# Kernel tuning notes

Hardware: AMD Instinct MI355X
Metric: run time of the kernel (lower is better)

Reference implementation:

```python
import jax, jax.numpy as jnp
import numpy as np

ALPHA = 0.2  # LeakyReLU negative slope


def _gat_layer(x, W, a):
    """One GraphAttentionLayer (concat=True -> elu output).
    x: (B,N,Din); W: (Din,F); a: (2F,1).
    Faithful to source: adj mask is computed then discarded (softmax over raw e),
    so adj does not enter the math. Uses the additive decomposition
    e_ij = leakyrelu(a1.h_i + a2.h_j) which is mathematically identical to the
    dense (N,N,2F) concat in the original.
    """
    h = x @ W                      # (B,N,F)
    F = W.shape[1]
    a1, a2 = a[:F, 0], a[F:, 0]    # (F,), (F,)
    f1 = h @ a1                    # (B,N)
    f2 = h @ a2                    # (B,N)
    e = jax.nn.leaky_relu(f1[:, :, None] + f2[:, None, :], negative_slope=ALPHA)  # (B,N,N)
    att = jax.nn.softmax(e, axis=-1)
    h_prime = jnp.einsum('bnm,bmf->bnf', att, h)
    return jax.nn.elu(h_prime)


def setup_inputs() -> dict:
    key = jax.random.key(0)
    ks = jax.random.split(key, 6)
    B, N, D, H, F = 8, 1024, 256, 8, 128
    x = jax.random.normal(ks[0], (B, N, D), jnp.float32)
    adj = (jax.random.uniform(ks[1], (N, N)) > 0.9).astype(jnp.float32)
    xavier = lambda fi, fo: 1.414 * (2.0 / (fi + fo)) ** 0.5
    W_heads = jax.random.normal(ks[2], (H, D, F), jnp.float32) * xavier(D, F)
    a_heads = jax.random.normal(ks[3], (H, 2 * F, 1), jnp.float32) * xavier(2 * F, 1)
    W_out = jax.random.normal(ks[4], (H * F, F), jnp.float32) * xavier(H * F, F)
    a_out = jax.random.normal(ks[5], (2 * F, 1), jnp.float32) * xavier(2 * F, 1)
    return {"x": x, "adj": adj, "W_heads": W_heads, "a_heads": a_heads,
            "W_out": W_out, "a_out": a_out}


def reference(x, adj, W_heads, a_heads, W_out, a_out):
    # GAT.forward (dropout omitted: eval mode identity). adj unused per source bug.
    heads = jax.vmap(lambda W, a: _gat_layer(x, W, a))(W_heads, a_heads)  # (H,B,N,F)
    B, N = x.shape[0], x.shape[1]
    xc = jnp.transpose(heads, (1, 2, 0, 3)).reshape(B, N, -1)  # concat heads: (B,N,H*F)
    # out_att has concat=True (applies elu), then GAT.forward applies elu again.
    return jax.nn.elu(_gat_layer(xc, W_out, a_out))
```

## Files before the change

kernel.cpp:

```cpp
#include <hip/hip_runtime.h>
#include <math.h>

#define ALPHA 0.2f
#define LOG2E 1.44269504089f

typedef __attribute__((ext_vector_type(8))) short bf16x8;
typedef __attribute__((ext_vector_type(4))) float f32x4;

__device__ __forceinline__ float elu1(float x)  { return x > 0.f ? x : (__expf(x) - 1.f); }

__device__ __forceinline__ unsigned short f2bf(float x) {
    unsigned u = __float_as_uint(x);
    return (unsigned short)((u + 0x7fffu + ((u >> 16) & 1u)) >> 16);
}
__device__ __forceinline__ unsigned pkbf16(float a, float b) {
    return (unsigned)f2bf(a) | ((unsigned)f2bf(b) << 16);
}
__device__ __forceinline__ float bflo(unsigned v) { return __uint_as_float(v << 16); }
__device__ __forceinline__ float bfhi(unsigned v) { return __uint_as_float(v & 0xffff0000u); }
__device__ __forceinline__ float bfs(unsigned short v) { return __uint_as_float((unsigned)v << 16); }
__device__ __forceinline__ unsigned pkbf_rhu(float a, float b) {
    unsigned ua = __float_as_uint(a) + 0x8000u;
    unsigned ub = __float_as_uint(b) + 0x8000u;
    return __builtin_amdgcn_perm(ub, ua, 0x07060302u);
}

__global__ __launch_bounds__(256) void cvt_w_all(
    const float* __restrict__ Wh, const float* __restrict__ Wo,
    unsigned short* __restrict__ WhT, unsigned short* __restrict__ WoT)
{
    const int z = blockIdx.z;
    const int K = (z < 8) ? 256 : 1024;
    if (blockIdx.x * 64 >= K) return;
    const float* in = (z < 8) ? (Wh + (size_t)z * K * 128) : Wo;
    unsigned short* out = (z < 8) ? (WhT + (size_t)z * 128 * K) : WoT;

    __shared__ float T[64][65];
    const int tid = threadIdx.x;
    const int k0 = blockIdx.x * 64, n0 = blockIdx.y * 64;

    const int kr = tid >> 4, nc = (tid & 15) * 4;
#pragma unroll
    for (int s = 0; s < 4; ++s) {
        float4 v = *(const float4*)(in + (size_t)(k0 + kr + s * 16) * 128 + n0 + nc);
        T[kr + s * 16][nc]     = v.x;
        T[kr + s * 16][nc + 1] = v.y;
        T[kr + s * 16][nc + 2] = v.z;
        T[kr + s * 16][nc + 3] = v.w;
    }
    __syncthreads();
    const int nr0 = tid >> 3, kc = (tid & 7) * 8;
#pragma unroll
    for (int s = 0; s < 2; ++s) {
        int nr = nr0 + s * 32;
        unsigned pk[4];
#pragma unroll
        for (int q = 0; q < 4; ++q)
            pk[q] = pkbf16(T[kc + 2 * q][nr], T[kc + 2 * q + 1][nr]);
        *(uint4*)(out + (size_t)(n0 + nr) * K + k0 + kc) = make_uint4(pk[0], pk[1], pk[2], pk[3]);
    }
}

template <int BM, int BN, int WM, int WN, int DOF, int AF32>
__global__ __launch_bounds__(256) void gemm_t(
    const void* __restrict__ Avp, const unsigned short* __restrict__ Bt,
    unsigned short* __restrict__ Ct, int K,
    const float* __restrict__ aV, float* __restrict__ f1g, float* __restrict__ f2g)
{
    const int RM = WM / 16, RN = WN / 16;
    const int NCA = BM * 8 / 256, NCB = BN * 8 / 256;
    __shared__ __align__(16) unsigned short SAB[(BM + BN) * 72];
    unsigned short (*As)[72] = (unsigned short(*)[72])SAB;
    unsigned short (*Bs)[72] = (unsigned short(*)[72])(SAB + BM * 72);
    unsigned short (*Cs)[BM + 8] = (unsigned short(*)[BM + 8])SAB;
    float* redf = (float*)(SAB + BN * (BM + 8));

    const int tid = threadIdx.x;
    const int w = tid >> 6, lane = tid & 63;
    const int n16 = lane & 15, quad = lane >> 4;
    const int WX = BM / WM;
    const int wm = (w % WX) * WM, wn = (w / WX) * WN;
    const int m0 = blockIdx.x * BM, n0 = blockIdx.y * BN;

    const float* Af = (const float*)Avp;
    const unsigned short* Ab = (const unsigned short*)Avp;
    const int ar = tid >> 2, akc = (tid & 3) * 16;

    f32x4 acc[RM][RN];
#pragma unroll
    for (int mm = 0; mm < RM; ++mm)
#pragma unroll
        for (int nn = 0; nn < RN; ++nn) acc[mm][nn] = (f32x4){0.f, 0.f, 0.f, 0.f};

    uint4 ra[NCA], rb[NCB];
    float4 raf[4];
    if (AF32) {
#pragma unroll
        for (int j = 0; j < 4; ++j)
            raf[j] = *(const float4*)(Af + (size_t)(m0 + ar) * K + akc + 4 * j);
    } else {
#pragma unroll
        for (int i = 0; i < NCA; ++i) {
            int c = tid * NCA + i, r = c >> 3, cc = (c & 7) * 8;
            ra[i] = *(const uint4*)(Ab + (size_t)(m0 + r) * K + cc);
        }
    }
#pragma unroll
    for (int i = 0; i < NCB; ++i) {
        int c = tid * NCB + i, r = c >> 3, cc = (c & 7) * 8;
        rb[i] = *(const uint4*)(Bt + (size_t)(n0 + r) * K + cc);
    }

    const int nk = K >> 6;
    for (int kt = 0; kt < nk; ++kt) {
        __syncthreads();
        if (AF32) {
            uint4 lo = make_uint4(pkbf16(raf[0].x, raf[0].y), pkbf16(raf[0].z, raf[0].w),
                                  pkbf16(raf[1].x, raf[1].y), pkbf16(raf[1].z, raf[1].w));
            uint4 hi = make_uint4(pkbf16(raf[2].x, raf[2].y), pkbf16(raf[2].z, raf[2].w),
                                  pkbf16(raf[3].x, raf[3].y), pkbf16(raf[3].z, raf[3].w));
            *(uint4*)&As[ar][akc]     = lo;
            *(uint4*)&As[ar][akc + 8] = hi;
        } else {
#pragma unroll
            for (int i = 0; i < NCA; ++i) {
                int c = tid * NCA + i, r = c >> 3, cc = (c & 7) * 8;
                *(uint4*)&As[r][cc] = ra[i];
            }
        }
#pragma unroll
        for (int i = 0; i < NCB; ++i) {
            int c = tid * NCB + i, r = c >> 3, cc = (c & 7) * 8;
            *(uint4*)&Bs[r][cc] = rb[i];
        }
        __syncthreads();
        if (kt + 1 < nk) {
            int k0 = (kt + 1) * 64;
            if (AF32) {
#pragma unroll
                for (int j = 0; j < 4; ++j)
                    raf[j] = *(const float4*)(Af + (size_t)(m0 + ar) * K + k0 + akc + 4 * j);
            } else {
#pragma unroll
                for (int i = 0; i < NCA; ++i) {
                    int c = tid * NCA + i, r = c >> 3, cc = (c & 7) * 8;
                    ra[i] = *(const uint4*)(Ab + (size_t)(m0 + r) * K + k0 + cc);
                }
            }
#pragma unroll
            for (int i = 0; i < NCB; ++i) {
                int c = tid * NCB + i, r = c >> 3, cc = (c & 7) * 8;
                rb[i] = *(const uint4*)(Bt + (size_t)(n0 + r) * K + k0 + cc);
            }
        }
#pragma unroll
        for (int ks = 0; ks < 2; ++ks) {
            bf16x8 am[RM], bn[RN];
#pragma unroll
            for (int mm = 0; mm < RM; ++mm)
                am[mm] = *(const bf16x8*)&As[wm + mm * 16 + n16][ks * 32 + quad * 8];
#pragma unroll
            for (int nn = 0; nn < RN; ++nn)
                bn[nn] = *(const bf16x8*)&Bs[wn + nn * 16 + n16][ks * 32 + quad * 8];
#pragma unroll
            for (int mm = 0; mm < RM; ++mm)
#pragma unroll
                for (int nn = 0; nn < RN; ++nn)
                    acc[mm][nn] = __builtin_amdgcn_mfma_f32_16x16x32_bf16(
                        am[mm], bn[nn], acc[mm][nn], 0, 0, 0);
        }
    }

    __syncthreads();

#pragma unroll
    for (int nn = 0; nn < RN; ++nn) {
        int n = wn + nn * 16 + n16;
#pragma unroll
        for (int mm = 0; mm < RM; ++mm) {
            int m = wm + mm * 16 + quad * 4;
            f32x4 a = acc[mm][nn];
            ushort4 o = make_ushort4(f2bf(a[0]), f2bf(a[1]), f2bf(a[2]), f2bf(a[3]));
            *(ushort4*)&Cs[n][m] = o;
        }
    }
    __syncthreads();

    const int CHUNKS = BM * 2 / 16;
    const int RPP = 256 / CHUNKS;
    const int row = tid / CHUNKS, ch = tid % CHUNKS;
#pragma unroll
    for (int s = 0; s < BN / RPP; ++s) {
        int n = row + s * RPP;
        *(uint4*)(Ct + (size_t)(n0 + n) * 8192 + m0 + ch * 8) =
            *(const uint4*)&Cs[n][ch * 8];
    }

    if (DOF) {
        const int G = 256 / BM;
        const int FP = 128 / G;
        const int mloc = tid % BM, fq = tid / BM;
        const float* az = aV + blockIdx.y * 256;
        float s1 = 0.f, s2 = 0.f;
#pragma unroll 8
        for (int k = 0; k < FP; ++k) {
            int f = fq * FP + k;
            float h = bfs(Cs[f][mloc]);
            s1 += h * az[f];
            s2 += h * az[128 + f];
        }
        *(float2*)&redf[(fq * BM + mloc) * 2] = make_float2(s1, s2);
        __syncthreads();
        if (tid < BM) {
            float a1 = 0.f, a2 = 0.f;
#pragma unroll
            for (int g = 0; g < G; ++g) {
                a1 += redf[(g * BM + tid) * 2];
                a2 += redf[(g * BM + tid) * 2 + 1];
            }
            f1g[(size_t)blockIdx.y * 8192 + m0 + tid] = a1;
            f2g[(size_t)blockIdx.y * 8192 + m0 + tid] = a2;
        }
    }
}

template <int NI, int OUTBF, int NT>
__global__ __launch_bounds__(256) void attn4(
    const unsigned short* __restrict__ hT, const float* __restrict__ f1g,
    const float* __restrict__ f2g, float* __restrict__ outf,
    unsigned short* __restrict__ outb, int elu2)
{
    const int N = 1024, JT = 64, JP = 72;
    __shared__ __align__(16) unsigned short hls[2][NT * 16][JP];
    __shared__ float ul[1024], vl[1024];
    __shared__ float wred[4];

    const int tid = threadIdx.x;
    const int w = tid >> 6, lane = tid & 63;
    const int n16 = lane & 15, quad = lane >> 4;
    const int hy = OUTBF ? blockIdx.x : 0;
    const int bz = OUTBF ? blockIdx.z : blockIdx.x;
    const int fz = OUTBF ? 0 : blockIdx.z;
    const int ibx = blockIdx.y;
    const int hb = hy * 8 + bz;
    const int ITILE = 64 * NI;
    const int iw0 = ibx * ITILE + w * (16 * NI);

    const int j4 = tid * 4;
    {
        float4 fv = *(const float4*)(f2g + (size_t)hb * N + j4);
        fv.x *= LOG2E; fv.y *= LOG2E; fv.z *= LOG2E; fv.w *= LOG2E;
        *(float4*)&ul[j4] = fv;
        float m4 = fmaxf(fmaxf(fv.x, fv.y), fmaxf(fv.z, fv.w));
#pragma unroll
        for (int off = 32; off; off >>= 1) m4 = fmaxf(m4, __shfl_xor(m4, off));
        if (lane == 0) wred[w] = m4;
    }

    float f1L[NI];
#pragma unroll
    for (int ii = 0; ii < NI; ++ii)
        f1L[ii] = f1g[(size_t)hb * N + iw0 + ii * 16 + n16] * LOG2E;

    const unsigned short* gsrc = hT + (size_t)(hy * 128 + fz * (NT * 16)) * 8192 + bz * 1024;
    const int sf = tid >> 3, sj = (tid & 7) * 8;

    bf16x8 stg[NT / 2];
#pragma unroll
    for (int s = 0; s < NT / 2; ++s)
        stg[s] = *(const bf16x8*)(gsrc + (size_t)(sf + 32 * s) * 8192 + sj);

    __syncthreads();
    const float f2mL = fmaxf(fmaxf(wred[0], wred[1]), fmaxf(wred[2], wred[3]));

    {
        float4 raw = *(const float4*)&ul[j4];
        float4 uu, vv;
        float d0 = raw.x - f2mL, d1 = raw.y - f2mL, d2 = raw.z - f2mL, d3 = raw.w - f2mL;
        uu.x = __builtin_amdgcn_exp2f(d0); vv.x = __builtin_amdgcn_exp2f(ALPHA * d0);
        uu.y = __builtin_amdgcn_exp2f(d1); vv.y = __builtin_amdgcn_exp2f(ALPHA * d1);
        uu.z = __builtin_amdgcn_exp2f(d2); vv.z = __builtin_amdgcn_exp2f(ALPHA * d2);
        uu.w = __builtin_amdgcn_exp2f(d3); vv.w = __builtin_amdgcn_exp2f(ALPHA * d3);
        *(float4*)&ul[j4] = uu;
        *(float4*)&vl[j4] = vv;
    }

    float ri[NI];
#pragma unroll
    for (int ii = 0; ii < NI; ++ii)
        ri[ii] = __builtin_amdgcn_exp2f((ALPHA - 1.f) * (f1L[ii] + f2mL));

    f32x4 acc[NI][NT], accl[NI];
#pragma unroll
    for (int ii = 0; ii < NI; ++ii) {
        accl[ii] = (f32x4){0.f, 0.f, 0.f, 0.f};
#pragma unroll
        for (int t = 0; t < NT; ++t) acc[ii][t] = (f32x4){0.f, 0.f, 0.f, 0.f};
    }
    bf16x8 ones;
    { union { bf16x8 v; unsigned u[4]; } o;
      o.u[0] = o.u[1] = o.u[2] = o.u[3] = 0x3F803F80u; ones = o.v; }

#pragma unroll
    for (int s = 0; s < NT / 2; ++s)
        *(bf16x8*)&hls[0][sf + 32 * s][sj] = stg[s];
    __syncthreads();

    for (int jt = 0; jt < N / JT; ++jt) {
        const int cur = jt & 1;
        if (jt + 1 < N / JT) {
            int j0n = (jt + 1) * JT;
#pragma unroll
            for (int s = 0; s < NT / 2; ++s)
                stg[s] = *(const bf16x8*)(gsrc + (size_t)(sf + 32 * s) * 8192 + j0n + sj);
        }
        const int j0 = jt * JT;
#pragma unroll
        for (int kk = 0; kk < 2; ++kk) {
            const int jb = j0 + kk * 32 + quad * 8;
            float4 u0 = *(const float4*)&ul[jb], u1 = *(const float4*)&ul[jb + 4];
            float4 v0 = *(const float4*)&vl[jb], v1 = *(const float4*)&vl[jb + 4];
            float uj[8] = {u0.x, u0.y, u0.z, u0.w, u1.x, u1.y, u1.z, u1.w};
            float vj[8] = {v0.x, v0.y, v0.z, v0.w, v1.x, v1.y, v1.z, v1.w};

            bf16x8 afr[NI];
#pragma unroll
            for (int ii = 0; ii < NI; ++ii) {
                union { bf16x8 v; unsigned u[4]; } cvt;
#pragma unroll
                for (int q = 0; q < 4; ++q) {
                    float p0 = fmaxf(uj[2 * q],     ri[ii] * vj[2 * q]);
                    float p1 = fmaxf(uj[2 * q + 1], ri[ii] * vj[2 * q + 1]);
                    cvt.u[q] = pkbf_rhu(p0, p1);
                }
                afr[ii] = cvt.v;
            }
#pragma unroll
            for (int t = 0; t < NT; ++t) {
                bf16x8 bfr = *(const bf16x8*)&hls[cur][t * 16 + n16][kk * 32 + quad * 8];
#pragma unroll
                for (int ii = 0; ii < NI; ++ii)
                    acc[ii][t] = __builtin_amdgcn_mfma_f32_16x16x32_bf16(
                        afr[ii], bfr, acc[ii][t], 0, 0, 0);
            }
#pragma unroll
            for (int ii = 0; ii < NI; ++ii)
                accl[ii] = __builtin_amdgcn_mfma_f32_16x16x32_bf16(
                    afr[ii], ones, accl[ii], 0, 0, 0);
        }
        if (jt + 1 < N / JT) {
#pragma unroll
            for (int s = 0; s < NT / 2; ++s)
                *(bf16x8*)&hls[1 - cur][sf + 32 * s][sj] = stg[s];
        }
        __syncthreads();
    }

#pragma unroll
    for (int ii = 0; ii < NI; ++ii) {
#pragma unroll
        for (int r = 0; r < 4; ++r) {
            float inv = 1.f / accl[ii][r];
            int i = iw0 + ii * 16 + quad * 4 + r;
#pragma unroll
            for (int t = 0; t < NT; ++t) {
                float tv = acc[ii][t][r] * inv;
                tv = elu1(tv);
                if (OUTBF) {
                    outb[(size_t)(bz * 1024 + i) * 1024 + hy * 128 + t * 16 + n16] = f2bf(tv);
                } else {
                    if (elu2) tv = elu1(tv);
                    outf[(size_t)(bz * 1024 + i) * 128 + fz * (NT * 16) + t * 16 + n16] = tv;
                }
            }
        }
    }
}

extern "C" void kernel_launch(void* const* d_in, const int* in_sizes, int n_in,
                              void* d_out, int out_size, void* d_ws, size_t ws_size,
                              hipStream_t stream)
{
    const float* x  = (const float*)d_in[0];
    const float* Wh = (const float*)d_in[2];
    const float* ah = (const float*)d_in[3];
    const float* Wo = (const float*)d_in[4];
    const float* ao = (const float*)d_in[5];
    float* out = (float*)d_out;

    unsigned short* WhT = (unsigned short*)d_ws;
    unsigned short* WoT = WhT + 262144;
    unsigned short* h1T = WoT + 131072;
    unsigned short* xcb = h1T + 8388608;
    unsigned short* h2T = xcb + 8388608;
    float* f1a  = (float*)(h2T + 1048576);
    float* f2a  = f1a + 65536;
    float* f1b  = f2a + 65536;
    float* f2b  = f1b + 8192;

    cvt_w_all<<<dim3(16, 2, 9), 256, 0, stream>>>(Wh, Wo, WhT, WoT);

    gemm_t<64, 128, 32, 64, 1, 1><<<dim3(128, 8), 256, 0, stream>>>(
        x, WhT, h1T, 256, ah, f1a, f2a);
    attn4<2, 1, 8><<<dim3(8, 8, 8), 256, 0, stream>>>(h1T, f1a, f2a, nullptr, xcb, 0);

    gemm_t<32, 128, 16, 64, 1, 0><<<dim3(256, 1), 256, 0, stream>>>(
        xcb, WoT, h2T, 1024, ao, f1b, f2b);
    attn4<1, 0, 4><<<dim3(8, 16, 2), 256, 0, stream>>>(h2T, f1b, f2b, out, nullptr, 1);
}
```

Before: 167.1 us.

## Pre-convert x to bf16, widen head attention blocks, stage bf16 output via LDS

The weight-conversion kernel now also converts x to bf16, so the first projection GEMM reads a bf16 input instead of fp32. The first attention kernel runs 512-thread blocks covering twice as many query rows. Each staged key/value tile is therefore reused across more rows, and the grid is halved. Its bf16 output is written through an LDS transpose buffer and stored as coalesced 16-byte rows instead of scattered 2-byte stores. The trade-offs are an extra global pass over x, larger blocks that may lower occupancy, and added block syncs in the epilogue.

```diff
diff --git a/kernel.cpp b/kernel.cpp
--- a/kernel.cpp
+++ b/kernel.cpp
@@ -27,16 +27,27 @@
 
 __global__ __launch_bounds__(256) void cvt_w_all(
     const float* __restrict__ Wh, const float* __restrict__ Wo,
-    unsigned short* __restrict__ WhT, unsigned short* __restrict__ WoT)
+    const float* __restrict__ xf,
+    unsigned short* __restrict__ WhT, unsigned short* __restrict__ WoT,
+    unsigned short* __restrict__ xbf)
 {
     const int z = blockIdx.z;
+    const int tid = threadIdx.x;
+    if (z >= 9) {
+        size_t idx = ((((size_t)(z - 9) * 2 + blockIdx.y) * 16) + blockIdx.x) * 2048
+                   + (size_t)tid * 8;
+        float4 a = *(const float4*)(xf + idx);
+        float4 b = *(const float4*)(xf + idx + 4);
+        *(uint4*)(xbf + idx) = make_uint4(pkbf16(a.x, a.y), pkbf16(a.z, a.w),
+                                          pkbf16(b.x, b.y), pkbf16(b.z, b.w));
+        return;
+    }
     const int K = (z < 8) ? 256 : 1024;
     if (blockIdx.x * 64 >= K) return;
     const float* in = (z < 8) ? (Wh + (size_t)z * K * 128) : Wo;
     unsigned short* out = (z < 8) ? (WhT + (size_t)z * 128 * K) : WoT;
 
     __shared__ float T[64][65];
-    const int tid = threadIdx.x;
     const int k0 = blockIdx.x * 64, n0 = blockIdx.y * 64;
 
     const int kr = tid >> 4, nc = (tid & 15) * 4;
@@ -224,16 +235,20 @@
     }
 }
 
-template <int NI, int OUTBF, int NT>
-__global__ __launch_bounds__(256) void attn4(
+template <int NI, int OUTBF, int NT, int THREADS>
+__global__ __launch_bounds__(THREADS) void attn4(
     const unsigned short* __restrict__ hT, const float* __restrict__ f1g,
     const float* __restrict__ f2g, float* __restrict__ outf,
     unsigned short* __restrict__ outb, int elu2)
 {
     const int N = 1024, JT = 64, JP = 72;
+    const int NW = THREADS / 64;
+    const int ITILE = 16 * NI * NW;
+    const int NTS = NT * 16 * 8 / THREADS;
+    const int SR = THREADS / 8;
     __shared__ __align__(16) unsigned short hls[2][NT * 16][JP];
     __shared__ float ul[1024], vl[1024];
-    __shared__ float wred[4];
+    __shared__ float wred[NW];
 
     const int tid = threadIdx.x;
     const int w = tid >> 6, lane = tid & 63;
@@ -243,11 +258,10 @@
     const int fz = OUTBF ? 0 : blockIdx.z;
     const int ibx = blockIdx.y;
     const int hb = hy * 8 + bz;
-    const int ITILE = 64 * NI;
     const int iw0 = ibx * ITILE + w * (16 * NI);
 
-    const int j4 = tid * 4;
-    {
+    if (THREADS == 256) {
+        const int j4 = tid * 4;
         float4 fv = *(const float4*)(f2g + (size_t)hb * N + j4);
         fv.x *= LOG2E; fv.y *= LOG2E; fv.z *= LOG2E; fv.w *= LOG2E;
         *(float4*)&ul[j4] = fv;
@@ -255,6 +269,15 @@
 #pragma unroll
         for (int off = 32; off; off >>= 1) m4 = fmaxf(m4, __shfl_xor(m4, off));
         if (lane == 0) wred[w] = m4;
+    } else {
+        const int j2 = tid * 2;
+        float2 fv = *(const float2*)(f2g + (size_t)hb * N + j2);
+        fv.x *= LOG2E; fv.y *= LOG2E;
+        *(float2*)&ul[j2] = fv;
+        float m4 = fmaxf(fv.x, fv.y);
+#pragma unroll
+        for (int off = 32; off; off >>= 1) m4 = fmaxf(m4, __shfl_xor(m4, off));
+        if (lane == 0) wred[w] = m4;
     }
 
     float f1L[NI];
@@ -265,15 +288,18 @@
     const unsigned short* gsrc = hT + (size_t)(hy * 128 + fz * (NT * 16)) * 8192 + bz * 1024;
     const int sf = tid >> 3, sj = (tid & 7) * 8;
 
-    bf16x8 stg[NT / 2];
-#pragma unroll
-    for (int s = 0; s < NT / 2; ++s)
-        stg[s] = *(const bf16x8*)(gsrc + (size_t)(sf + 32 * s) * 8192 + sj);
+    bf16x8 stg[NTS];
+#pragma unroll
+    for (int s = 0; s < NTS; ++s)
+        stg[s] = *(const bf16x8*)(gsrc + (size_t)(sf + SR * s) * 8192 + sj);
 
     __syncthreads();
-    const float f2mL = fmaxf(fmaxf(wred[0], wred[1]), fmaxf(wred[2], wred[3]));
-
-    {
+    float f2mL = wred[0];
+#pragma unroll
+    for (int k = 1; k < NW; ++k) f2mL = fmaxf(f2mL, wred[k]);
+
+    if (THREADS == 256) {
+        const int j4 = tid * 4;
         float4 raw = *(const float4*)&ul[j4];
         float4 uu, vv;
         float d0 = raw.x - f2mL, d1 = raw.y - f2mL, d2 = raw.z - f2mL, d3 = raw.w - f2mL;
@@ -283,6 +309,15 @@
         uu.w = __builtin_amdgcn_exp2f(d3); vv.w = __builtin_amdgcn_exp2f(ALPHA * d3);
         *(float4*)&ul[j4] = uu;
         *(float4*)&vl[j4] = vv;
+    } else {
+        const int j2 = tid * 2;
+        float2 raw = *(const float2*)&ul[j2];
+        float d0 = raw.x - f2mL, d1 = raw.y - f2mL;
+        float2 uu, vv;
+        uu.x = __builtin_amdgcn_exp2f(d0); vv.x = __builtin_amdgcn_exp2f(ALPHA * d0);
+        uu.y = __builtin_amdgcn_exp2f(d1); vv.y = __builtin_amdgcn_exp2f(ALPHA * d1);
+        *(float2*)&ul[j2] = uu;
+        *(float2*)&vl[j2] = vv;
     }
 
     float ri[NI];
@@ -302,8 +337,8 @@
       o.u[0] = o.u[1] = o.u[2] = o.u[3] = 0x3F803F80u; ones = o.v; }
 
 #pragma unroll
-    for (int s = 0; s < NT / 2; ++s)
-        *(bf16x8*)&hls[0][sf + 32 * s][sj] = stg[s];
+    for (int s = 0; s < NTS; ++s)
+        *(bf16x8*)&hls[0][sf + SR * s][sj] = stg[s];
     __syncthreads();
 
     for (int jt = 0; jt < N / JT; ++jt) {
@@ -311,8 +346,8 @@
         if (jt + 1 < N / JT) {
             int j0n = (jt + 1) * JT;
 #pragma unroll
-            for (int s = 0; s < NT / 2; ++s)
-                stg[s] = *(const bf16x8*)(gsrc + (size_t)(sf + 32 * s) * 8192 + j0n + sj);
+            for (int s = 0; s < NTS; ++s)
+                stg[s] = *(const bf16x8*)(gsrc + (size_t)(sf + SR * s) * 8192 + j0n + sj);
         }
         const int j0 = jt * JT;
 #pragma unroll
@@ -350,25 +385,56 @@
         }
         if (jt + 1 < N / JT) {
 #pragma unroll
-            for (int s = 0; s < NT / 2; ++s)
-                *(bf16x8*)&hls[1 - cur][sf + 32 * s][sj] = stg[s];
+            for (int s = 0; s < NTS; ++s)
+                *(bf16x8*)&hls[1 - cur][sf + SR * s][sj] = stg[s];
         }
         __syncthreads();
     }
 
-#pragma unroll
-    for (int ii = 0; ii < NI; ++ii) {
-#pragma unroll
-        for (int r = 0; r < 4; ++r) {
-            float inv = 1.f / accl[ii][r];
-            int i = iw0 + ii * 16 + quad * 4 + r;
-#pragma unroll
-            for (int t = 0; t < NT; ++t) {
-                float tv = acc[ii][t][r] * inv;
-                tv = elu1(tv);
-                if (OUTBF) {
-                    outb[(size_t)(bz * 1024 + i) * 1024 + hy * 128 + t * 16 + n16] = f2bf(tv);
-                } else {
+    if (OUTBF) {
+        unsigned short (*Os)[140] = (unsigned short(*)[140])hls;
+        const int WPP = 128 / (16 * NI);
+#pragma unroll
+        for (int pass = 0; pass < ITILE / 128; ++pass) {
+            __syncthreads();
+            if ((w / WPP) == pass) {
+#pragma unroll
+                for (int ii = 0; ii < NI; ++ii)
+#pragma unroll
+                    for (int r = 0; r < 4; ++r) {
+                        float inv = 1.f / accl[ii][r];
+                        int il = (w % WPP) * (16 * NI) + ii * 16 + quad * 4 + r;
+#pragma unroll
+                        for (int t = 0; t < NT; ++t)
+                            Os[il][t * 16 + n16] = f2bf(elu1(acc[ii][t][r] * inv));
+                    }
+            }
+            __syncthreads();
+            {
+                int orow = tid >> 2, q4 = tid & 3;
+                size_t gb = (size_t)(bz * 1024 + ibx * ITILE + pass * 128 + orow) * 1024
+                          + hy * 128 + q4 * 32;
+                uint2 d[8];
+#pragma unroll
+                for (int s = 0; s < 8; ++s)
+                    d[s] = *(const uint2*)&Os[orow][q4 * 32 + s * 4];
+                *(uint4*)(outb + gb)      = make_uint4(d[0].x, d[0].y, d[1].x, d[1].y);
+                *(uint4*)(outb + gb + 8)  = make_uint4(d[2].x, d[2].y, d[3].x, d[3].y);
+                *(uint4*)(outb + gb + 16) = make_uint4(d[4].x, d[4].y, d[5].x, d[5].y);
+                *(uint4*)(outb + gb + 24) = make_uint4(d[6].x, d[6].y, d[7].x, d[7].y);
+            }
+        }
+    } else {
+#pragma unroll
+        for (int ii = 0; ii < NI; ++ii) {
+#pragma unroll
+            for (int r = 0; r < 4; ++r) {
+                float inv = 1.f / accl[ii][r];
+                int i = iw0 + ii * 16 + quad * 4 + r;
+#pragma unroll
+                for (int t = 0; t < NT; ++t) {
+                    float tv = acc[ii][t][r] * inv;
+                    tv = elu1(tv);
                     if (elu2) tv = elu1(tv);
                     outf[(size_t)(bz * 1024 + i) * 128 + fz * (NT * 16) + t * 16 + n16] = tv;
                 }
@@ -397,14 +463,15 @@
     float* f2a  = f1a + 65536;
     float* f1b  = f2a + 65536;
     float* f2b  = f1b + 8192;
-
-    cvt_w_all<<<dim3(16, 2, 9), 256, 0, stream>>>(Wh, Wo, WhT, WoT);
-
-    gemm_t<64, 128, 32, 64, 1, 1><<<dim3(128, 8), 256, 0, stream>>>(
-        x, WhT, h1T, 256, ah, f1a, f2a);
-    attn4<2, 1, 8><<<dim3(8, 8, 8), 256, 0, stream>>>(h1T, f1a, f2a, nullptr, xcb, 0);
+    unsigned short* xbf = (unsigned short*)(f2b + 8192);
+
+    cvt_w_all<<<dim3(16, 2, 41), 256, 0, stream>>>(Wh, Wo, x, WhT, WoT, xbf);
+
+    gemm_t<64, 128, 32, 64, 1, 0><<<dim3(128, 8), 256, 0, stream>>>(
+        xbf, WhT, h1T, 256, ah, f1a, f2a);
+    attn4<2, 1, 8, 512><<<dim3(8, 4, 8), 512, 0, stream>>>(h1T, f1a, f2a, nullptr, xcb, 0);
 
     gemm_t<32, 128, 16, 64, 1, 0><<<dim3(256, 1), 256, 0, stream>>>(
         xcb, WoT, h2T, 1024, ao, f1b, f2b);
-    attn4<1, 0, 4><<<dim3(8, 16, 2), 256, 0, stream>>>(h2T, f1b, f2b, out, nullptr, 1);
-}
+    attn4<1, 0, 4, 256><<<dim3(8, 16, 2), 256, 0, stream>>>(h2T, f1b, f2b, out, nullptr, 1);
+}
```

After: 181.0 us. 8.3% more time.

## Stage full 64-feature h slice in LDS and widen attention and GEMM blocks

Applied to the files above, without the earlier changes.

The attention kernel now loads the whole 64x1024 bf16 slice of h into LDS once (about 129 KB) and drops the double-buffered 64-column j-tile pipeline and its per-tile barriers. Each block covers 64 output features instead of 128 or 64, and the first layer uses 512-thread blocks with four i-rows per warp. The first GEMM also moves to 128x128 tiles with 512 threads. The goal is to remove per-tile sync and staging overhead and to reuse each h slice across more rows. In exchange, the large LDS footprint limits occupancy to about one block per CU, and the initial load is no longer overlapped with compute.

```diff
diff --git a/kernel.cpp b/kernel.cpp
--- a/kernel.cpp
+++ b/kernel.cpp
@@ -16,8 +16,6 @@
 __device__ __forceinline__ unsigned pkbf16(float a, float b) {
     return (unsigned)f2bf(a) | ((unsigned)f2bf(b) << 16);
 }
-__device__ __forceinline__ float bflo(unsigned v) { return __uint_as_float(v << 16); }
-__device__ __forceinline__ float bfhi(unsigned v) { return __uint_as_float(v & 0xffff0000u); }
 __device__ __forceinline__ float bfs(unsigned short v) { return __uint_as_float((unsigned)v << 16); }
 __device__ __forceinline__ unsigned pkbf_rhu(float a, float b) {
     unsigned ua = __float_as_uint(a) + 0x8000u;
@@ -61,15 +59,18 @@
     }
 }
 
-template <int BM, int BN, int WM, int WN, int DOF, int AF32>
-__global__ __launch_bounds__(256) void gemm_t(
+template <int BM, int BN, int WM, int WN, int DOF, int AF32, int THREADS>
+__global__ __launch_bounds__(THREADS) void gemm_t(
     const void* __restrict__ Avp, const unsigned short* __restrict__ Bt,
     unsigned short* __restrict__ Ct, int K,
     const float* __restrict__ aV, float* __restrict__ f1g, float* __restrict__ f2g)
 {
     const int RM = WM / 16, RN = WN / 16;
-    const int NCA = BM * 8 / 256, NCB = BN * 8 / 256;
-    __shared__ __align__(16) unsigned short SAB[(BM + BN) * 72];
+    const int NCA = BM * 8 / THREADS, NCB = BN * 8 / THREADS;
+    constexpr int SAB_A = (BM + BN) * 72;
+    constexpr int SAB_B = BN * (BM + 8) + THREADS * 4;
+    constexpr int SAB_SH = SAB_A > SAB_B ? SAB_A : SAB_B;
+    __shared__ __align__(16) unsigned short SAB[SAB_SH];
     unsigned short (*As)[72] = (unsigned short(*)[72])SAB;
     unsigned short (*Bs)[72] = (unsigned short(*)[72])(SAB + BM * 72);
     unsigned short (*Cs)[BM + 8] = (unsigned short(*)[BM + 8])SAB;
@@ -92,7 +93,7 @@
 #pragma unroll
         for (int nn = 0; nn < RN; ++nn) acc[mm][nn] = (f32x4){0.f, 0.f, 0.f, 0.f};
 
-    uint4 ra[NCA], rb[NCB];
+    uint4 ra[NCA ? NCA : 1], rb[NCB];
     float4 raf[4];
     if (AF32) {
 #pragma unroll
@@ -187,7 +188,7 @@
     __syncthreads();
 
     const int CHUNKS = BM * 2 / 16;
-    const int RPP = 256 / CHUNKS;
+    const int RPP = THREADS / CHUNKS;
     const int row = tid / CHUNKS, ch = tid % CHUNKS;
 #pragma unroll
     for (int s = 0; s < BN / RPP; ++s) {
@@ -197,7 +198,7 @@
     }
 
     if (DOF) {
-        const int G = 256 / BM;
+        const int G = THREADS / BM;
         const int FP = 128 / G;
         const int mloc = tid % BM, fq = tid / BM;
         const float* az = aV + blockIdx.y * 256;
@@ -224,30 +225,31 @@
     }
 }
 
-template <int NI, int OUTBF, int NT>
-__global__ __launch_bounds__(256) void attn4(
+template <int NI, int OUTBF, int THREADS>
+__global__ __launch_bounds__(THREADS) void attn6(
     const unsigned short* __restrict__ hT, const float* __restrict__ f1g,
     const float* __restrict__ f2g, float* __restrict__ outf,
-    unsigned short* __restrict__ outb, int elu2)
+    unsigned short* __restrict__ outb)
 {
-    const int N = 1024, JT = 64, JP = 72;
-    __shared__ __align__(16) unsigned short hls[2][NT * 16][JP];
+    const int N = 1024;
+    const int NW = THREADS / 64;
+    const int ITILE = NW * 16 * NI;
+    const int EPT = 1024 / THREADS;
+    __shared__ __align__(16) unsigned short hfull[64][1032];
     __shared__ float ul[1024], vl[1024];
-    __shared__ float wred[4];
+    __shared__ float wred[NW];
 
     const int tid = threadIdx.x;
     const int w = tid >> 6, lane = tid & 63;
     const int n16 = lane & 15, quad = lane >> 4;
-    const int hy = OUTBF ? blockIdx.x : 0;
-    const int bz = OUTBF ? blockIdx.z : blockIdx.x;
-    const int fz = OUTBF ? 0 : blockIdx.z;
-    const int ibx = blockIdx.y;
+    int hy, bz, ibx, fz;
+    if (OUTBF) { hy = blockIdx.x; ibx = blockIdx.y; bz = blockIdx.z >> 1; fz = blockIdx.z & 1; }
+    else       { hy = 0; bz = blockIdx.x; ibx = blockIdx.y; fz = blockIdx.z; }
     const int hb = hy * 8 + bz;
-    const int ITILE = 64 * NI;
     const int iw0 = ibx * ITILE + w * (16 * NI);
 
-    const int j4 = tid * 4;
-    {
+    if (EPT == 4) {
+        const int j4 = tid * 4;
         float4 fv = *(const float4*)(f2g + (size_t)hb * N + j4);
         fv.x *= LOG2E; fv.y *= LOG2E; fv.z *= LOG2E; fv.w *= LOG2E;
         *(float4*)&ul[j4] = fv;
@@ -255,6 +257,15 @@
 #pragma unroll
         for (int off = 32; off; off >>= 1) m4 = fmaxf(m4, __shfl_xor(m4, off));
         if (lane == 0) wred[w] = m4;
+    } else {
+        const int j2 = tid * 2;
+        float2 fv = *(const float2*)(f2g + (size_t)hb * N + j2);
+        fv.x *= LOG2E; fv.y *= LOG2E;
+        *(float2*)&ul[j2] = fv;
+        float m4 = fmaxf(fv.x, fv.y);
+#pragma unroll
+        for (int off = 32; off; off >>= 1) m4 = fmaxf(m4, __shfl_xor(m4, off));
+        if (lane == 0) wred[w] = m4;
     }
 
     float f1L[NI];
@@ -262,18 +273,24 @@
     for (int ii = 0; ii < NI; ++ii)
         f1L[ii] = f1g[(size_t)hb * N + iw0 + ii * 16 + n16] * LOG2E;
 
-    const unsigned short* gsrc = hT + (size_t)(hy * 128 + fz * (NT * 16)) * 8192 + bz * 1024;
-    const int sf = tid >> 3, sj = (tid & 7) * 8;
-
-    bf16x8 stg[NT / 2];
-#pragma unroll
-    for (int s = 0; s < NT / 2; ++s)
-        stg[s] = *(const bf16x8*)(gsrc + (size_t)(sf + 32 * s) * 8192 + sj);
+    const unsigned short* gsrc = hT + (size_t)(hy * 128 + fz * 64) * 8192 + bz * 1024;
+    const int sr = tid >> 3;
+    const int sc = (tid & 7) * 8;
+    const int SRW = THREADS / 8;
+#pragma unroll
+    for (int s = 0; s < 64 / SRW; ++s)
+#pragma unroll
+        for (int c = 0; c < 16; ++c)
+            *(bf16x8*)&hfull[sr + SRW * s][sc + c * 64] =
+                *(const bf16x8*)(gsrc + (size_t)(sr + SRW * s) * 8192 + sc + c * 64);
 
     __syncthreads();
-    const float f2mL = fmaxf(fmaxf(wred[0], wred[1]), fmaxf(wred[2], wred[3]));
-
-    {
+    float f2mL = wred[0];
+#pragma unroll
+    for (int k = 1; k < NW; ++k) f2mL = fmaxf(f2mL, wred[k]);
+
+    if (EPT == 4) {
+        const int j4 = tid * 4;
         float4 raw = *(const float4*)&ul[j4];
         float4 uu, vv;
         float d0 = raw.x - f2mL, d1 = raw.y - f2mL, d2 = raw.z - f2mL, d3 = raw.w - f2mL;
@@ -283,6 +300,15 @@
         uu.w = __builtin_amdgcn_exp2f(d3); vv.w = __builtin_amdgcn_exp2f(ALPHA * d3);
         *(float4*)&ul[j4] = uu;
         *(float4*)&vl[j4] = vv;
+    } else {
+        const int j2 = tid * 2;
+        float2 raw = *(const float2*)&ul[j2];
+        float d0 = raw.x - f2mL, d1 = raw.y - f2mL;
+        float2 uu, vv;
+        uu.x = __builtin_amdgcn_exp2f(d0); vv.x = __builtin_amdgcn_exp2f(ALPHA * d0);
+        uu.y = __builtin_amdgcn_exp2f(d1); vv.y = __builtin_amdgcn_exp2f(ALPHA * d1);
+        *(float2*)&ul[j2] = uu;
+        *(float2*)&vl[j2] = vv;
     }
 
     float ri[NI];
@@ -290,70 +316,50 @@
     for (int ii = 0; ii < NI; ++ii)
         ri[ii] = __builtin_amdgcn_exp2f((ALPHA - 1.f) * (f1L[ii] + f2mL));
 
-    f32x4 acc[NI][NT], accl[NI];
+    f32x4 acc[NI][4], accl[NI];
 #pragma unroll
     for (int ii = 0; ii < NI; ++ii) {
         accl[ii] = (f32x4){0.f, 0.f, 0.f, 0.f};
 #pragma unroll
-        for (int t = 0; t < NT; ++t) acc[ii][t] = (f32x4){0.f, 0.f, 0.f, 0.f};
+        for (int t = 0; t < 4; ++t) acc[ii][t] = (f32x4){0.f, 0.f, 0.f, 0.f};
     }
     bf16x8 ones;
     { union { bf16x8 v; unsigned u[4]; } o;
       o.u[0] = o.u[1] = o.u[2] = o.u[3] = 0x3F803F80u; ones = o.v; }
 
-#pragma unroll
-    for (int s = 0; s < NT / 2; ++s)
-        *(bf16x8*)&hls[0][sf + 32 * s][sj] = stg[s];
     __syncthreads();
 
-    for (int jt = 0; jt < N / JT; ++jt) {
-        const int cur = jt & 1;
-        if (jt + 1 < N / JT) {
-            int j0n = (jt + 1) * JT;
-#pragma unroll
-            for (int s = 0; s < NT / 2; ++s)
-                stg[s] = *(const bf16x8*)(gsrc + (size_t)(sf + 32 * s) * 8192 + j0n + sj);
-        }
-        const int j0 = jt * JT;
-#pragma unroll
-        for (int kk = 0; kk < 2; ++kk) {
-            const int jb = j0 + kk * 32 + quad * 8;
-            float4 u0 = *(const float4*)&ul[jb], u1 = *(const float4*)&ul[jb + 4];
-            float4 v0 = *(const float4*)&vl[jb], v1 = *(const float4*)&vl[jb + 4];
-            float uj[8] = {u0.x, u0.y, u0.z, u0.w, u1.x, u1.y, u1.z, u1.w};
-            float vj[8] = {v0.x, v0.y, v0.z, v0.w, v1.x, v1.y, v1.z, v1.w};
-
-            bf16x8 afr[NI];
-#pragma unroll
-            for (int ii = 0; ii < NI; ++ii) {
-                union { bf16x8 v; unsigned u[4]; } cvt;
-#pragma unroll
-                for (int q = 0; q < 4; ++q) {
-                    float p0 = fmaxf(uj[2 * q],     ri[ii] * vj[2 * q]);
-                    float p1 = fmaxf(uj[2 * q + 1], ri[ii] * vj[2 * q + 1]);
-                    cvt.u[q] = pkbf_rhu(p0, p1);
-                }
-                afr[ii] = cvt.v;
-            }
-#pragma unroll
-            for (int t = 0; t < NT; ++t) {
-                bf16x8 bfr = *(const bf16x8*)&hls[cur][t * 16 + n16][kk * 32 + quad * 8];
-#pragma unroll
-                for (int ii = 0; ii < NI; ++ii)
-                    acc[ii][t] = __builtin_amdgcn_mfma_f32_16x16x32_bf16(
-                        afr[ii], bfr, acc[ii][t], 0, 0, 0);
-            }
+    for (int kk = 0; kk < 32; ++kk) {
+        const int jb = kk * 32 + quad * 8;
+        float4 u0 = *(const float4*)&ul[jb], u1 = *(const float4*)&ul[jb + 4];
+        float4 v0 = *(const float4*)&vl[jb], v1 = *(const float4*)&vl[jb + 4];
+        float uj[8] = {u0.x, u0.y, u0.z, u0.w, u1.x, u1.y, u1.z, u1.w};
+        float vj[8] = {v0.x, v0.y, v0.z, v0.w, v1.x, v1.y, v1.z, v1.w};
+
+        bf16x8 afr[NI];
+#pragma unroll
+        for (int ii = 0; ii < NI; ++ii) {
+            union { bf16x8 v; unsigned u[4]; } cvt;
+#pragma unroll
+            for (int q = 0; q < 4; ++q) {
+                float p0 = fmaxf(uj[2 * q],     ri[ii] * vj[2 * q]);
+                float p1 = fmaxf(uj[2 * q + 1], ri[ii] * vj[2 * q + 1]);
+                cvt.u[q] = pkbf_rhu(p0, p1);
+            }
+            afr[ii] = cvt.v;
+        }
+#pragma unroll
+        for (int t = 0; t < 4; ++t) {
+            bf16x8 bfr = *(const bf16x8*)&hfull[t * 16 + n16][jb];
 #pragma unroll
             for (int ii = 0; ii < NI; ++ii)
-                accl[ii] = __builtin_amdgcn_mfma_f32_16x16x32_bf16(
-                    afr[ii], ones, accl[ii], 0, 0, 0);
-        }
-        if (jt + 1 < N / JT) {
-#pragma unroll
-            for (int s = 0; s < NT / 2; ++s)
-                *(bf16x8*)&hls[1 - cur][sf + 32 * s][sj] = stg[s];
-        }
-        __syncthreads();
+                acc[ii][t] = __builtin_amdgcn_mfma_f32_16x16x32_bf16(
+                    afr[ii], bfr, acc[ii][t], 0, 0, 0);
+        }
+#pragma unroll
+        for (int ii = 0; ii < NI; ++ii)
+            accl[ii] = __builtin_amdgcn_mfma_f32_16x16x32_bf16(
+                afr[ii], ones, accl[ii], 0, 0, 0);
     }
 
 #pragma unroll
@@ -363,14 +369,15 @@
             float inv = 1.f / accl[ii][r];
             int i = iw0 + ii * 16 + quad * 4 + r;
 #pragma unroll
-            for (int t = 0; t < NT; ++t) {
+            for (int t = 0; t < 4; ++t) {
                 float tv = acc[ii][t][r] * inv;
                 tv = elu1(tv);
                 if (OUTBF) {
-                    outb[(size_t)(bz * 1024 + i) * 1024 + hy * 128 + t * 16 + n16] = f2bf(tv);
+                    outb[(size_t)(bz * 1024 + i) * 1024 + hy * 128 + fz * 64 + t * 16 + n16]
+                        = f2bf(tv);
                 } else {
-                    if (elu2) tv = elu1(tv);
-                    outf[(size_t)(bz * 1024 + i) * 128 + fz * (NT * 16) + t * 16 + n16] = tv;
+                    tv = elu1(tv);
+                    outf[(size_t)(bz * 1024 + i) * 128 + fz * 64 + t * 16 + n16] = tv;
                 }
             }
         }
@@ -400,11 +407,11 @@
 
     cvt_w_all<<<dim3(16, 2, 9), 256, 0, stream>>>(Wh, Wo, WhT, WoT);
 
-    gemm_t<64, 128, 32, 64, 1, 1><<<dim3(128, 8), 256, 0, stream>>>(
+    gemm_t<128, 128, 32, 64, 1, 1, 512><<<dim3(64, 8), 512, 0, stream>>>(
         x, WhT, h1T, 256, ah, f1a, f2a);
-    attn4<2, 1, 8><<<dim3(8, 8, 8), 256, 0, stream>>>(h1T, f1a, f2a, nullptr, xcb, 0);
-
-    gemm_t<32, 128, 16, 64, 1, 0><<<dim3(256, 1), 256, 0, stream>>>(
+    attn6<4, 1, 512><<<dim3(8, 2, 16), 512, 0, stream>>>(h1T, f1a, f2a, nullptr, xcb);
+
+    gemm_t<32, 128, 16, 64, 1, 0, 256><<<dim3(256, 1), 256, 0, stream>>>(
         xcb, WoT, h2T, 1024, ao, f1b, f2b);
-    attn4<1, 0, 4><<<dim3(8, 16, 2), 256, 0, stream>>>(h2T, f1b, f2b, out, nullptr, 1);
-}
+    attn6<1, 0, 256><<<dim3(8, 16, 2), 256, 0, stream>>>(h2T, f1b, f2b, out, nullptr);
+}
```

Result: faster. 158.6 us (-5.1%).
